# Kernel tuning notes

Measured on AMD Instinct MI355X. Metric: run time of the kernel, lower is better.

The kernel has to match this reference:

```python
import jax, jax.numpy as jnp
import numpy as np

POOL = 7
SUB = 2
C = 256
NUM_CLASS = 81
N_ROIS = 1000
IMG = 1024


def _roi_align(feat, rois, img_size, pool=POOL, sub=SUB):
    # feat: (1, C, H, W); rois: (N, 4) as (y1, x1, y2, x2) in image coords
    H, W = feat.shape[2], feat.shape[3]
    fhw = jnp.array([H, W, H, W], jnp.float32) - 1.0
    im = jnp.concatenate([img_size, img_size]).astype(jnp.float32) - 1.0
    rif = rois * fhw / im  # rois mapped into feature-map coords
    S = pool * sub  # subsampled grid per axis (14)
    h_step = (rif[:, 2] - rif[:, 0]) / S  # (N,)
    w_step = (rif[:, 3] - rif[:, 1]) / S
    grid = jnp.arange(S, dtype=jnp.float32) + 0.5
    ys = grid[None, :] * h_step[:, None] + rif[:, 0:1]  # (N, S)
    xs = grid[None, :] * w_step[:, None] + rif[:, 1:2]  # (N, S)
    cy = ys[:, :, None]  # (N, S, 1) -> broadcast (N, S, S)
    cx = xs[:, None, :]  # (N, 1, S)
    iu = jnp.floor(cy)
    il = jnp.floor(cx)
    ly = cy - iu  # frac parts (bilinear weights)
    lx = cx - il
    iu = iu.astype(jnp.int32)
    il = il.astype(jnp.int32)
    idn = jnp.ceil(cy).astype(jnp.int32)
    ir = jnp.ceil(cx).astype(jnp.int32)
    iu = jnp.broadcast_to(iu, (rois.shape[0], S, S))
    idn = jnp.broadcast_to(idn, (rois.shape[0], S, S))
    il = jnp.broadcast_to(il, (rois.shape[0], S, S))
    ir = jnp.broadcast_to(ir, (rois.shape[0], S, S))
    f = feat[0]  # (C, H, W)
    # fancy-index gather of 4 corners: each (C, N, S, S)
    pre = (f[:, iu, il] * (1 - ly) * (1 - lx)
           + f[:, idn, il] * ly * (1 - lx)
           + f[:, iu, ir] * (1 - ly) * lx
           + f[:, idn, ir] * ly * lx)
    pre = pre.transpose(1, 0, 2, 3)  # (N, C, S, S)
    N = rois.shape[0]
    post = pre.reshape(N, f.shape[0], pool, sub, pool, sub).max(axis=(3, 5))
    return post  # (N, C, pool, pool)


def _pyramid_roi_pool(feats, rois, img_size):
    h = rois[:, 2] - rois[:, 0] + 1
    w = rois[:, 3] - rois[:, 1] + 1
    lvl = jnp.floor(jnp.log(jnp.sqrt(h * w) / 224.0) / 0.693147 + 4.0)
    lvl = jnp.clip(lvl, 2.0, 5.0)
    # compute ROIAlign against each level, select per-roi by mask
    out = jnp.zeros((rois.shape[0], C, POOL, POOL), jnp.float32)
    for i, l in enumerate(range(2, 6)):
        pooled = _roi_align(feats[i], rois, img_size)
        mask = (lvl == l)[:, None, None, None]
        out = jnp.where(mask, pooled, out)
    return out


def setup_inputs() -> dict:
    key = jax.random.key(0)
    ks = jax.random.split(key, 10)
    feat2 = jax.random.normal(ks[0], (1, C, 256, 256), jnp.float32)
    feat3 = jax.random.normal(ks[1], (1, C, 128, 128), jnp.float32)
    feat4 = jax.random.normal(ks[2], (1, C, 64, 64), jnp.float32)
    feat5 = jax.random.normal(ks[3], (1, C, 32, 32), jnp.float32)
    # valid boxes: log-uniform sizes in [32, 512] to cover levels 2..5
    u = jax.random.uniform(ks[4], (N_ROIS, 4))
    sh = jnp.exp(jnp.log(32.0) + u[:, 0] * (jnp.log(512.0) - jnp.log(32.0)))
    sw = jnp.exp(jnp.log(32.0) + u[:, 1] * (jnp.log(512.0) - jnp.log(32.0)))
    y1 = u[:, 2] * (IMG - 1 - sh)
    x1 = u[:, 3] * (IMG - 1 - sw)
    rois = jnp.stack([y1, x1, y1 + sh, x1 + sw], axis=1).astype(jnp.float32)
    img_size = jnp.array([IMG, IMG], jnp.int32)
    D = C * POOL * POOL  # 12544
    W1 = jax.random.normal(ks[5], (D, 1024), jnp.float32) * 0.01
    b1 = jnp.zeros((1024,), jnp.float32)
    W2 = jax.random.normal(ks[6], (1024, 1024), jnp.float32) * 0.01
    b2 = jnp.zeros((1024,), jnp.float32)
    Wloc = jax.random.normal(ks[7], (1024, NUM_CLASS * 4), jnp.float32) * 0.001
    bloc = jnp.zeros((NUM_CLASS * 4,), jnp.float32)
    Wsc = jax.random.normal(ks[8], (1024, NUM_CLASS), jnp.float32) * 0.01
    bsc = jnp.zeros((NUM_CLASS,), jnp.float32)
    return {"feat2": feat2, "feat3": feat3, "feat4": feat4, "feat5": feat5,
            "rois": rois, "img_size": img_size,
            "W1": W1, "b1": b1, "W2": W2, "b2": b2,
            "Wloc": Wloc, "bloc": bloc, "Wsc": Wsc, "bsc": bsc}


def reference(feat2, feat3, feat4, feat5, rois, img_size,
              W1, b1, W2, b2, Wloc, bloc, Wsc, bsc):
    pooled = _pyramid_roi_pool([feat2, feat3, feat4, feat5], rois, img_size)
    x = pooled.reshape(pooled.shape[0], -1)  # (N, 12544)
    fc = jax.nn.relu(x @ W1 + b1)
    fc = jax.nn.relu(fc @ W2 + b2)
    roi_cls_locs = fc @ Wloc + bloc
    roi_scores = fc @ Wsc + bsc
    return roi_cls_locs, roi_scores
```

## Files before the change

kernel.cpp:

```cpp
#include <hip/hip_runtime.h>
#include <hip/hip_bf16.h>
#include <cstdint>
#include <cstddef>

typedef __bf16 bf16x8 __attribute__((ext_vector_type(8)));
typedef _Float16 f16x8 __attribute__((ext_vector_type(8)));
typedef _Float16 f16x4 __attribute__((ext_vector_type(4)));
typedef float floatx4 __attribute__((ext_vector_type(4)));

#define NROIS 1000
#define PD    12544
#define K2_2  2048
#define NLOC  324
#define NSC   81
#define NH    405

#define OFF_T2    0u
#define OFF_T3    16777216u
#define OFF_T4    20971520u
#define OFF_T5    22020096u
#define OFF_FT    0u
#define OFF_POOL  11141120u
#define OFF_W1T   17563648u
#define OFF_PART1 23986176u
#define OFF_FC1   32374784u
#define OFF_W2T   33423360u
#define OFF_WHT   34471936u
#define OFF_FC2   34996224u
#define OFF_PART2 23986176u

__device__ __forceinline__ unsigned short f2bf(float x) {
    unsigned int u = __float_as_uint(x);
    u = u + 0x7fffu + ((u >> 16) & 1u);
    return (unsigned short)(u >> 16);
}
__device__ __forceinline__ float bf2f(unsigned short h) {
    return __uint_as_float(((unsigned int)h) << 16);
}
__device__ __forceinline__ ushort2 split_hl(float f) {
    const unsigned short hi = f2bf(f);
    const unsigned short lo = f2bf(f - bf2f(hi));
    return make_ushort2(hi, lo);
}

__global__ __launch_bounds__(256) void prep_kernel(
    const float* __restrict__ f2, const float* __restrict__ f3,
    const float* __restrict__ f4, const float* __restrict__ f5,
    _Float16* __restrict__ fT,
    const float* __restrict__ W1, _Float16* __restrict__ W1T,
    const float* __restrict__ W2, const float* __restrict__ Wloc,
    const float* __restrict__ Wsc, ushort2* __restrict__ W2T,
    ushort2* __restrict__ WhT)
{
    __shared__ float tile[64][65];
    const int bid = blockIdx.x;
    const int tid = threadIdx.x;
    const int g4  = tid & 15;
    const int pr  = tid >> 4;

    if (bid < 5440) {
        int bx = bid % 1360;
        const int c0 = (bid / 1360) * 64;
        const float* src; _Float16* dst; int P;
        if (bx < 1024)      {            src = f2; dst = fT + OFF_T2; P = 65536; }
        else if (bx < 1280) { bx -= 1024; src = f3; dst = fT + OFF_T3; P = 16384; }
        else if (bx < 1344) { bx -= 1280; src = f4; dst = fT + OFF_T4; P = 4096; }
        else                { bx -= 1344; src = f5; dst = fT + OFF_T5; P = 1024; }
        const int p0 = bx * 64;

#pragma unroll
        for (int k = 0; k < 4; ++k) {
            const int ch = pr + k * 16;
            const float4 v = *reinterpret_cast<const float4*>(
                &src[(size_t)(c0 + ch) * P + p0 + g4 * 4]);
            tile[ch][g4 * 4 + 0] = v.x;
            tile[ch][g4 * 4 + 1] = v.y;
            tile[ch][g4 * 4 + 2] = v.z;
            tile[ch][g4 * 4 + 3] = v.w;
        }
        __syncthreads();

#pragma unroll
        for (int k = 0; k < 4; ++k) {
            const int px = pr + k * 16;
            union { _Float16 h[4]; uint2 u; } pk;
            pk.h[0] = (_Float16)tile[g4 * 4 + 0][px];
            pk.h[1] = (_Float16)tile[g4 * 4 + 1][px];
            pk.h[2] = (_Float16)tile[g4 * 4 + 2][px];
            pk.h[3] = (_Float16)tile[g4 * 4 + 3][px];
            *reinterpret_cast<uint2*>(&dst[(size_t)(p0 + px) * 256 + c0 + g4 * 4]) = pk.u;
        }
    } else if (bid < 8576) {
        const int v  = bid - 5440;
        const int p0 = (v % 196) * 64;
        const int n0 = (v / 196) * 64;

#pragma unroll
        for (int k = 0; k < 4; ++k) {
            const int r    = pr + k * 16;
            const int pp   = p0 + r;
            const int ksrc = (pp & 255) * 49 + (pp >> 8);
            const float4 w = *reinterpret_cast<const float4*>(
                &W1[(size_t)ksrc * 1024 + n0 + g4 * 4]);
            tile[r][g4 * 4 + 0] = w.x;
            tile[r][g4 * 4 + 1] = w.y;
            tile[r][g4 * 4 + 2] = w.z;
            tile[r][g4 * 4 + 3] = w.w;
        }
        __syncthreads();

#pragma unroll
        for (int k = 0; k < 4; ++k) {
            const int nr = pr + k * 16;
            union { _Float16 h[4]; uint2 u; } pk;
            pk.h[0] = (_Float16)tile[g4 * 4 + 0][nr];
            pk.h[1] = (_Float16)tile[g4 * 4 + 1][nr];
            pk.h[2] = (_Float16)tile[g4 * 4 + 2][nr];
            pk.h[3] = (_Float16)tile[g4 * 4 + 3][nr];
            *reinterpret_cast<uint2*>(&W1T[(size_t)(n0 + nr) * PD + p0 + g4 * 4]) = pk.u;
        }
    } else {
        const int v  = bid - 8576;
        const int p0 = (v % 16) * 64;
        const int by = v / 16;
        const int col = tid & 63;
        const int r0  = tid >> 6;

        if (by < 16) {
            const int n0 = by * 64;
#pragma unroll
            for (int k = 0; k < 4; ++k) {
                const int r = pr + k * 16;
                const float4 w = *reinterpret_cast<const float4*>(
                    &W2[(size_t)(p0 + r) * 1024 + n0 + g4 * 4]);
                tile[r][g4 * 4 + 0] = w.x;
                tile[r][g4 * 4 + 1] = w.y;
                tile[r][g4 * 4 + 2] = w.z;
                tile[r][g4 * 4 + 3] = w.w;
            }
            __syncthreads();
#pragma unroll
            for (int nr = r0; nr < 64; nr += 4)
                W2T[(size_t)(n0 + nr) * 1024 + p0 + col] = split_hl(tile[col][nr]);
        } else {
            const int n0 = (by - 16) * 64;
#pragma unroll
            for (int r = r0; r < 64; r += 4) {
                const int pp = p0 + r;
                const int n  = n0 + col;
                float w = 0.0f;
                if (n < NLOC)    w = Wloc[(size_t)pp * NLOC + n];
                else if (n < NH) w = Wsc[(size_t)pp * NSC + (n - NLOC)];
                tile[r][col] = w;
            }
            __syncthreads();
#pragma unroll
            for (int nr = r0; nr < 64; nr += 4)
                WhT[(size_t)(n0 + nr) * 1024 + p0 + col] = split_hl(tile[col][nr]);
        }
    }
}

__global__ __launch_bounds__(256) void roi_pool_kernel(
    const _Float16* __restrict__ fT, const float* __restrict__ rois,
    const int* __restrict__ img_size, _Float16* __restrict__ pooledH)
{
    const int roi  = blockIdx.x;
    const int ph   = blockIdx.y;
    const int tid  = threadIdx.x;
    const int lane = tid & 63;
    const int wave = tid >> 6;
    const int syy  = wave >> 1;
    const int sxp  = wave & 1;

    const float y1 = rois[roi * 4 + 0];
    const float x1 = rois[roi * 4 + 1];
    const float y2 = rois[roi * 4 + 2];
    const float x2 = rois[roi * 4 + 3];

    const float hh = y2 - y1 + 1.0f;
    const float ww = x2 - x1 + 1.0f;
    float lvlf = floorf(logf(sqrtf(hh * ww) / 224.0f) / 0.693147f + 4.0f);
    lvlf = fminf(fmaxf(lvlf, 2.0f), 5.0f);
    const int lvl = (int)lvlf;

    const _Float16* f;
    int H;
    if (lvl == 2)      { f = fT + OFF_T2; H = 256; }
    else if (lvl == 3) { f = fT + OFF_T3; H = 128; }
    else if (lvl == 4) { f = fT + OFF_T4; H = 64;  }
    else               { f = fT + OFF_T5; H = 32;  }
    const int W = H;

    const float imh = (float)img_size[0] - 1.0f;
    const float imw = (float)img_size[1] - 1.0f;
    const float r0 = y1 * (float)(H - 1) / imh;
    const float r1 = x1 * (float)(W - 1) / imw;
    const float r2 = y2 * (float)(H - 1) / imh;
    const float r3 = x2 * (float)(W - 1) / imw;
    const float hs  = (r2 - r0) * (1.0f / 14.0f);
    const float wst = (r3 - r1) * (1.0f / 14.0f);

    const float cy = ((float)(ph * 2 + syy) + 0.5f) * hs + r0;
    const float fy = floorf(cy);
    int   iu  = (int)fy;
    int   idn = (int)ceilf(cy);
    const float ly = cy - fy;
    iu  = min(max(iu, 0),  H - 1);
    idn = min(max(idn, 0), H - 1);
    const float wU = 1.0f - ly, wD = ly;
    const f16x4* rowU = (const f16x4*)(f + (size_t)(iu  * W) * 256);
    const f16x4* rowD = (const f16x4*)(f + (size_t)(idn * W) * 256);

    __shared__ float4 red[4][7][64];

#pragma unroll
    for (int pw = 0; pw < 7; ++pw) {
        const int sx = pw * 2 + sxp;
        const float cx = ((float)sx + 0.5f) * wst + r1;
        const float fx = floorf(cx);
        int   il = (int)fx;
        int   ir = (int)ceilf(cx);
        const float lx = cx - fx;
        il = min(max(il, 0), W - 1);
        ir = min(max(ir, 0), W - 1);

        const f16x4 h00 = rowU[il * 64 + lane];
        const f16x4 h01 = rowU[ir * 64 + lane];
        const f16x4 h10 = rowD[il * 64 + lane];
        const f16x4 h11 = rowD[ir * 64 + lane];
        const float lxm = 1.0f - lx;
        float4 v;
        v.x = ((float)h00.x * lxm + (float)h01.x * lx) * wU + ((float)h10.x * lxm + (float)h11.x * lx) * wD;
        v.y = ((float)h00.y * lxm + (float)h01.y * lx) * wU + ((float)h10.y * lxm + (float)h11.y * lx) * wD;
        v.z = ((float)h00.z * lxm + (float)h01.z * lx) * wU + ((float)h10.z * lxm + (float)h11.z * lx) * wD;
        v.w = ((float)h00.w * lxm + (float)h01.w * lx) * wU + ((float)h10.w * lxm + (float)h11.w * lx) * wD;
        red[wave][pw][lane] = v;
    }
    __syncthreads();

    for (int idx = tid; idx < 448; idx += 256) {
        const int pw = idx >> 6, cg = idx & 63;
        const float4 a = red[0][pw][cg];
        const float4 b = red[1][pw][cg];
        const float4 c = red[2][pw][cg];
        const float4 d = red[3][pw][cg];
        union { _Float16 h[4]; uint2 v2; } pk;
        pk.h[0] = (_Float16)fmaxf(fmaxf(a.x, b.x), fmaxf(c.x, d.x));
        pk.h[1] = (_Float16)fmaxf(fmaxf(a.y, b.y), fmaxf(c.y, d.y));
        pk.h[2] = (_Float16)fmaxf(fmaxf(a.z, b.z), fmaxf(c.z, d.z));
        pk.h[3] = (_Float16)fmaxf(fmaxf(a.w, b.w), fmaxf(c.w, d.w));
        _Float16* outp = pooledH + (size_t)roi * PD + (ph * 7 + pw) * 256 + cg * 4;
        *reinterpret_cast<uint2*>(outp) = pk.v2;
    }
}

template<bool F16>
__global__ __launch_bounds__(256, 4) void gemm_16b_kernel(
    const unsigned short* __restrict__ A,
    const unsigned short* __restrict__ B,
    float* __restrict__ partial,
    int K2, int N)
{
    __shared__ __align__(16) unsigned short As[64 * 64];
    __shared__ __align__(16) unsigned short Bs[128 * 64];

    const int tid  = threadIdx.x;
    const int lane = tid & 63;
    const int wave = tid >> 6;

    const int totalSteps = K2 >> 6;
    const int nz = gridDim.x;
    const int z  = blockIdx.x;
    const int q  = totalSteps / nz, r = totalSteps % nz;
    const int myStart = z * q + min(z, r);
    const int mySteps = q + (z < r ? 1 : 0);

    const int n0 = blockIdx.y * 128;
    const int m0 = blockIdx.z * 64;

    const int rIn  = lane >> 3;
    const int cSrc = (lane & 7) ^ rIn;

    const int mrow = lane & 15, quad = lane >> 4;

    floatx4 acc[8];
#pragma unroll
    for (int j = 0; j < 8; ++j)
        acc[j] = (floatx4){0.f, 0.f, 0.f, 0.f};

    for (int s = 0; s < mySteps; ++s) {
        const int k0 = (myStart + s) * 64;
#pragma unroll
        for (int qq = 0; qq < 2; ++qq) {
            const int rowBase = wave * 16 + qq * 8;
            const unsigned short* ga =
                A + (size_t)(m0 + rowBase + rIn) * K2 + k0 + cSrc * 8;
            __builtin_amdgcn_global_load_lds(
                (const __attribute__((address_space(1))) void*)ga,
                (__attribute__((address_space(3))) void*)&As[rowBase * 64], 16, 0, 0);
        }
#pragma unroll
        for (int qq = 0; qq < 4; ++qq) {
            const int rowBase = wave * 32 + qq * 8;
            const unsigned short* gb =
                B + (size_t)(n0 + rowBase + rIn) * K2 + k0 + cSrc * 8;
            __builtin_amdgcn_global_load_lds(
                (const __attribute__((address_space(1))) void*)gb,
                (__attribute__((address_space(3))) void*)&Bs[rowBase * 64], 16, 0, 0);
        }
        __syncthreads();

#pragma unroll
        for (int ks = 0; ks < 2; ++ks) {
            const int ra = wave * 16 + mrow;
            const int ca = ((ks * 4 + quad) ^ (ra & 7)) * 8;
#pragma unroll
            for (int j = 0; j < 8; ++j) {
                const int rb = j * 16 + mrow;
                const int cb = ((ks * 4 + quad) ^ (rb & 7)) * 8;
                if constexpr (F16) {
                    const f16x8 aF = *reinterpret_cast<const f16x8*>(&As[ra * 64 + ca]);
                    const f16x8 bF = *reinterpret_cast<const f16x8*>(&Bs[rb * 64 + cb]);
                    acc[j] = __builtin_amdgcn_mfma_f32_16x16x32_f16(aF, bF, acc[j], 0, 0, 0);
                } else {
                    const bf16x8 aF = *reinterpret_cast<const bf16x8*>(&As[ra * 64 + ca]);
                    const bf16x8 bF = *reinterpret_cast<const bf16x8*>(&Bs[rb * 64 + cb]);
                    acc[j] = __builtin_amdgcn_mfma_f32_16x16x32_bf16(aF, bF, acc[j], 0, 0, 0);
                }
            }
        }
        __syncthreads();
    }

    float* p = partial + (size_t)blockIdx.x * (size_t)(gridDim.z * 64) * N;
    const int row = m0 + wave * 16 + quad * 4;
#pragma unroll
    for (int j = 0; j < 8; ++j) {
        const int col = n0 + j * 16 + mrow;
#pragma unroll
        for (int rr = 0; rr < 4; ++rr)
            p[(size_t)(row + rr) * N + col] = acc[j][rr];
    }
}

__global__ __launch_bounds__(256) void reduce_fc_kernel(
    const float* __restrict__ partial, const float* __restrict__ bias,
    ushort2* __restrict__ outHL, int nz)
{
    const int i4 = blockIdx.x * 256 + threadIdx.x;
    const int off = i4 * 4;
    const int m = off >> 10, n = off & 1023;
    float4 acc = *reinterpret_cast<const float4*>(partial + off);
    for (int z = 1; z < nz; ++z) {
        const float4 v = *reinterpret_cast<const float4*>(
            partial + (size_t)z * 1024 * 1024 + off);
        acc.x += v.x; acc.y += v.y; acc.z += v.z; acc.w += v.w;
    }
    const float4 bv = *reinterpret_cast<const float4*>(bias + n);
    ushort2* o = outHL + (size_t)m * 1024 + n;
    o[0] = split_hl(fmaxf(acc.x + bv.x, 0.f));
    o[1] = split_hl(fmaxf(acc.y + bv.y, 0.f));
    o[2] = split_hl(fmaxf(acc.z + bv.z, 0.f));
    o[3] = split_hl(fmaxf(acc.w + bv.w, 0.f));
}

__global__ __launch_bounds__(256) void reduce_heads_kernel(
    const float* __restrict__ partial, const float* __restrict__ bloc,
    const float* __restrict__ bsc, float* __restrict__ out0,
    float* __restrict__ out1, int nz)
{
    const int m = blockIdx.x;
    for (int n = threadIdx.x; n < NH; n += 256) {
        float s = 0.f;
        for (int z = 0; z < nz; ++z)
            s += partial[(size_t)z * 1024 * 512 + (size_t)m * 512 + n];
        if (n < NLOC) out0[(size_t)m * NLOC + n] = s + bloc[n];
        else          out1[(size_t)m * NSC + (n - NLOC)] = s + bsc[n - NLOC];
    }
}

extern "C" void kernel_launch(void* const* d_in, const int* in_sizes, int n_in,
                              void* d_out, int out_size, void* d_ws, size_t ws_size,
                              hipStream_t stream)
{
    const float* f2   = (const float*)d_in[0];
    const float* f3   = (const float*)d_in[1];
    const float* f4   = (const float*)d_in[2];
    const float* f5   = (const float*)d_in[3];
    const float* rois = (const float*)d_in[4];
    const int*   img  = (const int*)d_in[5];
    const float* W1   = (const float*)d_in[6];
    const float* b1   = (const float*)d_in[7];
    const float* W2   = (const float*)d_in[8];
    const float* b2   = (const float*)d_in[9];
    const float* Wloc = (const float*)d_in[10];
    const float* bloc = (const float*)d_in[11];
    const float* Wsc  = (const float*)d_in[12];
    const float* bsc  = (const float*)d_in[13];
    float* out = (float*)d_out;

    float* ws = (float*)d_ws;
    _Float16*  fT     = (_Float16*)(ws + OFF_FT);
    _Float16*  pooled = (_Float16*)(ws + OFF_POOL);
    _Float16*  w1t    = (_Float16*)(ws + OFF_W1T);
    float*     part1  = ws + OFF_PART1;
    float*     part2  = ws + OFF_PART2;
    ushort2*   w2t    = (ushort2*)(ws + OFF_W2T);
    ushort2*   wht    = (ushort2*)(ws + OFF_WHT);
    ushort2*   fc1    = (ushort2*)(ws + OFF_FC1);
    ushort2*   fc2    = (ushort2*)(ws + OFF_FC2);

    prep_kernel<<<dim3(8944), 256, 0, stream>>>(
        f2, f3, f4, f5, fT, W1, w1t, W2, Wloc, Wsc, w2t, wht);

    roi_pool_kernel<<<dim3(NROIS, 7), 256, 0, stream>>>(fT, rois, img, pooled);

    gemm_16b_kernel<true><<<dim3(8, 8, 16), 256, 0, stream>>>(
        (const unsigned short*)pooled, (const unsigned short*)w1t, part1,
        PD, 1024);
    reduce_fc_kernel<<<1024, 256, 0, stream>>>(part1, b1, fc1, 8);

    gemm_16b_kernel<false><<<dim3(4, 8, 16), 256, 0, stream>>>(
        (const unsigned short*)fc1, (const unsigned short*)w2t, part2,
        K2_2, 1024);
    reduce_fc_kernel<<<1024, 256, 0, stream>>>(part2, b2, fc2, 4);

    gemm_16b_kernel<false><<<dim3(8, 4, 16), 256, 0, stream>>>(
        (const unsigned short*)fc2, (const unsigned short*)wht, part2,
        K2_2, 512);
    reduce_heads_kernel<<<NROIS, 256, 0, stream>>>(
        part2, bloc, bsc, out, out + (size_t)NROIS * NLOC, 8);
}
```

Before: 312.7 us.

## Use plain fp16 for FC2/heads and co-schedule weight prep with ROI pooling

FC2 and the head GEMMs switch from split hi/lo bf16 operands (K doubled to 2048) to single fp16 operands with K=1024. That halves the MFMA work and the weight and activation bytes for those GEMMs. The weight-transpose work now runs in the same launch as the ROI pooling blocks, and only the feature transpose stays in its own kernel, so weight prep overlaps pooling. The cost is lower accuracy, since the compensated split-precision scheme is gone and fp16 range limits now apply to the activations and weights.

```diff
diff --git a/kernel.cpp b/kernel.cpp
--- a/kernel.cpp
+++ b/kernel.cpp
@@ -3,14 +3,13 @@
 #include <cstdint>
 #include <cstddef>
 
-typedef __bf16 bf16x8 __attribute__((ext_vector_type(8)));
 typedef _Float16 f16x8 __attribute__((ext_vector_type(8)));
 typedef _Float16 f16x4 __attribute__((ext_vector_type(4)));
 typedef float floatx4 __attribute__((ext_vector_type(4)));
 
 #define NROIS 1000
 #define PD    12544
-#define K2_2  2048
+#define KFC   1024
 #define NLOC  324
 #define NSC   81
 #define NH    405
@@ -24,110 +23,189 @@
 #define OFF_W1T   17563648u
 #define OFF_PART1 23986176u
 #define OFF_FC1   32374784u
-#define OFF_W2T   33423360u
-#define OFF_WHT   34471936u
-#define OFF_FC2   34996224u
+#define OFF_W2T   32899072u
+#define OFF_WHT   33423360u
+#define OFF_FC2   33685504u
 #define OFF_PART2 23986176u
 
-__device__ __forceinline__ unsigned short f2bf(float x) {
-    unsigned int u = __float_as_uint(x);
-    u = u + 0x7fffu + ((u >> 16) & 1u);
-    return (unsigned short)(u >> 16);
-}
-__device__ __forceinline__ float bf2f(unsigned short h) {
-    return __uint_as_float(((unsigned int)h) << 16);
-}
-__device__ __forceinline__ ushort2 split_hl(float f) {
-    const unsigned short hi = f2bf(f);
-    const unsigned short lo = f2bf(f - bf2f(hi));
-    return make_ushort2(hi, lo);
-}
-
-__global__ __launch_bounds__(256) void prep_kernel(
+__global__ __launch_bounds__(256) void transpose_feat_kernel(
     const float* __restrict__ f2, const float* __restrict__ f3,
     const float* __restrict__ f4, const float* __restrict__ f5,
-    _Float16* __restrict__ fT,
-    const float* __restrict__ W1, _Float16* __restrict__ W1T,
-    const float* __restrict__ W2, const float* __restrict__ Wloc,
-    const float* __restrict__ Wsc, ushort2* __restrict__ W2T,
-    ushort2* __restrict__ WhT)
+    _Float16* __restrict__ fT)
 {
     __shared__ float tile[64][65];
-    const int bid = blockIdx.x;
     const int tid = threadIdx.x;
     const int g4  = tid & 15;
     const int pr  = tid >> 4;
 
-    if (bid < 5440) {
-        int bx = bid % 1360;
-        const int c0 = (bid / 1360) * 64;
-        const float* src; _Float16* dst; int P;
-        if (bx < 1024)      {            src = f2; dst = fT + OFF_T2; P = 65536; }
-        else if (bx < 1280) { bx -= 1024; src = f3; dst = fT + OFF_T3; P = 16384; }
-        else if (bx < 1344) { bx -= 1280; src = f4; dst = fT + OFF_T4; P = 4096; }
-        else                { bx -= 1344; src = f5; dst = fT + OFF_T5; P = 1024; }
-        const int p0 = bx * 64;
-
-#pragma unroll
-        for (int k = 0; k < 4; ++k) {
-            const int ch = pr + k * 16;
-            const float4 v = *reinterpret_cast<const float4*>(
-                &src[(size_t)(c0 + ch) * P + p0 + g4 * 4]);
-            tile[ch][g4 * 4 + 0] = v.x;
-            tile[ch][g4 * 4 + 1] = v.y;
-            tile[ch][g4 * 4 + 2] = v.z;
-            tile[ch][g4 * 4 + 3] = v.w;
+    int bx = blockIdx.x % 1360;
+    const int c0 = (blockIdx.x / 1360) * 64;
+    const float* src; _Float16* dst; int P;
+    if (bx < 1024)      {            src = f2; dst = fT + OFF_T2; P = 65536; }
+    else if (bx < 1280) { bx -= 1024; src = f3; dst = fT + OFF_T3; P = 16384; }
+    else if (bx < 1344) { bx -= 1280; src = f4; dst = fT + OFF_T4; P = 4096; }
+    else                { bx -= 1344; src = f5; dst = fT + OFF_T5; P = 1024; }
+    const int p0 = bx * 64;
+
+#pragma unroll
+    for (int k = 0; k < 4; ++k) {
+        const int ch = pr + k * 16;
+        const float4 v = *reinterpret_cast<const float4*>(
+            &src[(size_t)(c0 + ch) * P + p0 + g4 * 4]);
+        tile[ch][g4 * 4 + 0] = v.x;
+        tile[ch][g4 * 4 + 1] = v.y;
+        tile[ch][g4 * 4 + 2] = v.z;
+        tile[ch][g4 * 4 + 3] = v.w;
+    }
+    __syncthreads();
+#pragma unroll
+    for (int k = 0; k < 4; ++k) {
+        const int px = pr + k * 16;
+        union { _Float16 h[4]; uint2 u; } pk;
+        pk.h[0] = (_Float16)tile[g4 * 4 + 0][px];
+        pk.h[1] = (_Float16)tile[g4 * 4 + 1][px];
+        pk.h[2] = (_Float16)tile[g4 * 4 + 2][px];
+        pk.h[3] = (_Float16)tile[g4 * 4 + 3][px];
+        *reinterpret_cast<uint2*>(&dst[(size_t)(p0 + px) * 256 + c0 + g4 * 4]) = pk.u;
+    }
+}
+
+__global__ __launch_bounds__(256) void pool_prep_kernel(
+    const _Float16* __restrict__ fT, const float* __restrict__ rois,
+    const int* __restrict__ img_size, _Float16* __restrict__ pooledH,
+    const float* __restrict__ W1, _Float16* __restrict__ W1T,
+    const float* __restrict__ W2, const float* __restrict__ Wloc,
+    const float* __restrict__ Wsc, _Float16* __restrict__ W2T,
+    _Float16* __restrict__ WhT)
+{
+    __shared__ __align__(16) char smem[28672];
+    const int bid = blockIdx.x;
+    const int tid = threadIdx.x;
+
+    if (bid < 7000) {
+        const int roi  = bid / 7;
+        const int ph   = bid % 7;
+        const int lane = tid & 63;
+        const int wave = tid >> 6;
+        const int syy  = wave >> 1;
+        const int sxp  = wave & 1;
+
+        const float y1 = rois[roi * 4 + 0];
+        const float x1 = rois[roi * 4 + 1];
+        const float y2 = rois[roi * 4 + 2];
+        const float x2 = rois[roi * 4 + 3];
+
+        const float hh = y2 - y1 + 1.0f;
+        const float ww = x2 - x1 + 1.0f;
+        float lvlf = floorf(logf(sqrtf(hh * ww) / 224.0f) / 0.693147f + 4.0f);
+        lvlf = fminf(fmaxf(lvlf, 2.0f), 5.0f);
+        const int lvl = (int)lvlf;
+
+        const _Float16* f;
+        int H;
+        if (lvl == 2)      { f = fT + OFF_T2; H = 256; }
+        else if (lvl == 3) { f = fT + OFF_T3; H = 128; }
+        else if (lvl == 4) { f = fT + OFF_T4; H = 64;  }
+        else               { f = fT + OFF_T5; H = 32;  }
+        const int W = H;
+
+        const float imh = (float)img_size[0] - 1.0f;
+        const float imw = (float)img_size[1] - 1.0f;
+        const float r0 = y1 * (float)(H - 1) / imh;
+        const float r1 = x1 * (float)(W - 1) / imw;
+        const float r2 = y2 * (float)(H - 1) / imh;
+        const float r3 = x2 * (float)(W - 1) / imw;
+        const float hs  = (r2 - r0) * (1.0f / 14.0f);
+        const float wst = (r3 - r1) * (1.0f / 14.0f);
+
+        const float cy = ((float)(ph * 2 + syy) + 0.5f) * hs + r0;
+        const float fy = floorf(cy);
+        int   iu  = (int)fy;
+        int   idn = (int)ceilf(cy);
+        const float ly = cy - fy;
+        iu  = min(max(iu, 0),  H - 1);
+        idn = min(max(idn, 0), H - 1);
+        const float wU = 1.0f - ly, wD = ly;
+        const f16x4* rowU = (const f16x4*)(f + (size_t)(iu  * W) * 256);
+        const f16x4* rowD = (const f16x4*)(f + (size_t)(idn * W) * 256);
+
+        float4 (*red)[7][64] = reinterpret_cast<float4 (*)[7][64]>(smem);
+
+#pragma unroll
+        for (int pw = 0; pw < 7; ++pw) {
+            const int sx = pw * 2 + sxp;
+            const float cx = ((float)sx + 0.5f) * wst + r1;
+            const float fx = floorf(cx);
+            int   il = (int)fx;
+            int   ir = (int)ceilf(cx);
+            const float lx = cx - fx;
+            il = min(max(il, 0), W - 1);
+            ir = min(max(ir, 0), W - 1);
+
+            const f16x4 h00 = rowU[il * 64 + lane];
+            const f16x4 h01 = rowU[ir * 64 + lane];
+            const f16x4 h10 = rowD[il * 64 + lane];
+            const f16x4 h11 = rowD[ir * 64 + lane];
+            const float lxm = 1.0f - lx;
+            float4 v;
+            v.x = ((float)h00.x * lxm + (float)h01.x * lx) * wU + ((float)h10.x * lxm + (float)h11.x * lx) * wD;
+            v.y = ((float)h00.y * lxm + (float)h01.y * lx) * wU + ((float)h10.y * lxm + (float)h11.y * lx) * wD;
+            v.z = ((float)h00.z * lxm + (float)h01.z * lx) * wU + ((float)h10.z * lxm + (float)h11.z * lx) * wD;
+            v.w = ((float)h00.w * lxm + (float)h01.w * lx) * wU + ((float)h10.w * lxm + (float)h11.w * lx) * wD;
+            red[wave][pw][lane] = v;
         }
         __syncthreads();
 
-#pragma unroll
-        for (int k = 0; k < 4; ++k) {
-            const int px = pr + k * 16;
-            union { _Float16 h[4]; uint2 u; } pk;
-            pk.h[0] = (_Float16)tile[g4 * 4 + 0][px];
-            pk.h[1] = (_Float16)tile[g4 * 4 + 1][px];
-            pk.h[2] = (_Float16)tile[g4 * 4 + 2][px];
-            pk.h[3] = (_Float16)tile[g4 * 4 + 3][px];
-            *reinterpret_cast<uint2*>(&dst[(size_t)(p0 + px) * 256 + c0 + g4 * 4]) = pk.u;
-        }
-    } else if (bid < 8576) {
-        const int v  = bid - 5440;
-        const int p0 = (v % 196) * 64;
-        const int n0 = (v / 196) * 64;
-
-#pragma unroll
-        for (int k = 0; k < 4; ++k) {
-            const int r    = pr + k * 16;
-            const int pp   = p0 + r;
-            const int ksrc = (pp & 255) * 49 + (pp >> 8);
-            const float4 w = *reinterpret_cast<const float4*>(
-                &W1[(size_t)ksrc * 1024 + n0 + g4 * 4]);
-            tile[r][g4 * 4 + 0] = w.x;
-            tile[r][g4 * 4 + 1] = w.y;
-            tile[r][g4 * 4 + 2] = w.z;
-            tile[r][g4 * 4 + 3] = w.w;
-        }
-        __syncthreads();
-
-#pragma unroll
-        for (int k = 0; k < 4; ++k) {
-            const int nr = pr + k * 16;
-            union { _Float16 h[4]; uint2 u; } pk;
-            pk.h[0] = (_Float16)tile[g4 * 4 + 0][nr];
-            pk.h[1] = (_Float16)tile[g4 * 4 + 1][nr];
-            pk.h[2] = (_Float16)tile[g4 * 4 + 2][nr];
-            pk.h[3] = (_Float16)tile[g4 * 4 + 3][nr];
-            *reinterpret_cast<uint2*>(&W1T[(size_t)(n0 + nr) * PD + p0 + g4 * 4]) = pk.u;
+        for (int idx = tid; idx < 448; idx += 256) {
+            const int pw = idx >> 6, cg = idx & 63;
+            const float4 a = red[0][pw][cg];
+            const float4 b = red[1][pw][cg];
+            const float4 c = red[2][pw][cg];
+            const float4 d = red[3][pw][cg];
+            union { _Float16 h[4]; uint2 v2; } pk;
+            pk.h[0] = (_Float16)fmaxf(fmaxf(a.x, b.x), fmaxf(c.x, d.x));
+            pk.h[1] = (_Float16)fmaxf(fmaxf(a.y, b.y), fmaxf(c.y, d.y));
+            pk.h[2] = (_Float16)fmaxf(fmaxf(a.z, b.z), fmaxf(c.z, d.z));
+            pk.h[3] = (_Float16)fmaxf(fmaxf(a.w, b.w), fmaxf(c.w, d.w));
+            _Float16* outp = pooledH + (size_t)roi * PD + (ph * 7 + pw) * 256 + cg * 4;
+            *reinterpret_cast<uint2*>(outp) = pk.v2;
         }
     } else {
-        const int v  = bid - 8576;
-        const int p0 = (v % 16) * 64;
-        const int by = v / 16;
-        const int col = tid & 63;
-        const int r0  = tid >> 6;
-
-        if (by < 16) {
-            const int n0 = by * 64;
+        float (*tile)[65] = reinterpret_cast<float (*)[65]>(smem);
+        const int g4 = tid & 15;
+        const int pr = tid >> 4;
+
+        if (bid < 10136) {
+            const int v  = bid - 7000;
+            const int p0 = (v % 196) * 64;
+            const int n0 = (v / 196) * 64;
+#pragma unroll
+            for (int k = 0; k < 4; ++k) {
+                const int r    = pr + k * 16;
+                const int pp   = p0 + r;
+                const int ksrc = (pp & 255) * 49 + (pp >> 8);
+                const float4 w = *reinterpret_cast<const float4*>(
+                    &W1[(size_t)ksrc * 1024 + n0 + g4 * 4]);
+                tile[r][g4 * 4 + 0] = w.x;
+                tile[r][g4 * 4 + 1] = w.y;
+                tile[r][g4 * 4 + 2] = w.z;
+                tile[r][g4 * 4 + 3] = w.w;
+            }
+            __syncthreads();
+#pragma unroll
+            for (int k = 0; k < 4; ++k) {
+                const int nr = pr + k * 16;
+                union { _Float16 h[4]; uint2 u; } pk;
+                pk.h[0] = (_Float16)tile[g4 * 4 + 0][nr];
+                pk.h[1] = (_Float16)tile[g4 * 4 + 1][nr];
+                pk.h[2] = (_Float16)tile[g4 * 4 + 2][nr];
+                pk.h[3] = (_Float16)tile[g4 * 4 + 3][nr];
+                *reinterpret_cast<uint2*>(&W1T[(size_t)(n0 + nr) * PD + p0 + g4 * 4]) = pk.u;
+            }
+        } else if (bid < 10392) {
+            const int v  = bid - 10136;
+            const int p0 = (v % 16) * 64;
+            const int n0 = (v / 16) * 64;
 #pragma unroll
             for (int k = 0; k < 4; ++k) {
                 const int r = pr + k * 16;
@@ -140,10 +218,21 @@
             }
             __syncthreads();
 #pragma unroll
-            for (int nr = r0; nr < 64; nr += 4)
-                W2T[(size_t)(n0 + nr) * 1024 + p0 + col] = split_hl(tile[col][nr]);
+            for (int k = 0; k < 4; ++k) {
+                const int nr = pr + k * 16;
+                union { _Float16 h[4]; uint2 u; } pk;
+                pk.h[0] = (_Float16)tile[g4 * 4 + 0][nr];
+                pk.h[1] = (_Float16)tile[g4 * 4 + 1][nr];
+                pk.h[2] = (_Float16)tile[g4 * 4 + 2][nr];
+                pk.h[3] = (_Float16)tile[g4 * 4 + 3][nr];
+                *reinterpret_cast<uint2*>(&W2T[(size_t)(n0 + nr) * KFC + p0 + g4 * 4]) = pk.u;
+            }
         } else {
-            const int n0 = (by - 16) * 64;
+            const int v  = bid - 10392;
+            const int p0 = (v % 16) * 64;
+            const int n0 = (v / 16) * 64;
+            const int col = tid & 63;
+            const int r0  = tid >> 6;
 #pragma unroll
             for (int r = r0; r < 64; r += 4) {
                 const int pp = p0 + r;
@@ -155,108 +244,20 @@
             }
             __syncthreads();
 #pragma unroll
-            for (int nr = r0; nr < 64; nr += 4)
-                WhT[(size_t)(n0 + nr) * 1024 + p0 + col] = split_hl(tile[col][nr]);
-        }
-    }
-}
-
-__global__ __launch_bounds__(256) void roi_pool_kernel(
-    const _Float16* __restrict__ fT, const float* __restrict__ rois,
-    const int* __restrict__ img_size, _Float16* __restrict__ pooledH)
-{
-    const int roi  = blockIdx.x;
-    const int ph   = blockIdx.y;
-    const int tid  = threadIdx.x;
-    const int lane = tid & 63;
-    const int wave = tid >> 6;
-    const int syy  = wave >> 1;
-    const int sxp  = wave & 1;
-
-    const float y1 = rois[roi * 4 + 0];
-    const float x1 = rois[roi * 4 + 1];
-    const float y2 = rois[roi * 4 + 2];
-    const float x2 = rois[roi * 4 + 3];
-
-    const float hh = y2 - y1 + 1.0f;
-    const float ww = x2 - x1 + 1.0f;
-    float lvlf = floorf(logf(sqrtf(hh * ww) / 224.0f) / 0.693147f + 4.0f);
-    lvlf = fminf(fmaxf(lvlf, 2.0f), 5.0f);
-    const int lvl = (int)lvlf;
-
-    const _Float16* f;
-    int H;
-    if (lvl == 2)      { f = fT + OFF_T2; H = 256; }
-    else if (lvl == 3) { f = fT + OFF_T3; H = 128; }
-    else if (lvl == 4) { f = fT + OFF_T4; H = 64;  }
-    else               { f = fT + OFF_T5; H = 32;  }
-    const int W = H;
-
-    const float imh = (float)img_size[0] - 1.0f;
-    const float imw = (float)img_size[1] - 1.0f;
-    const float r0 = y1 * (float)(H - 1) / imh;
-    const float r1 = x1 * (float)(W - 1) / imw;
-    const float r2 = y2 * (float)(H - 1) / imh;
-    const float r3 = x2 * (float)(W - 1) / imw;
-    const float hs  = (r2 - r0) * (1.0f / 14.0f);
-    const float wst = (r3 - r1) * (1.0f / 14.0f);
-
-    const float cy = ((float)(ph * 2 + syy) + 0.5f) * hs + r0;
-    const float fy = floorf(cy);
-    int   iu  = (int)fy;
-    int   idn = (int)ceilf(cy);
-    const float ly = cy - fy;
-    iu  = min(max(iu, 0),  H - 1);
-    idn = min(max(idn, 0), H - 1);
-    const float wU = 1.0f - ly, wD = ly;
-    const f16x4* rowU = (const f16x4*)(f + (size_t)(iu  * W) * 256);
-    const f16x4* rowD = (const f16x4*)(f + (size_t)(idn * W) * 256);
-
-    __shared__ float4 red[4][7][64];
-
-#pragma unroll
-    for (int pw = 0; pw < 7; ++pw) {
-        const int sx = pw * 2 + sxp;
-        const float cx = ((float)sx + 0.5f) * wst + r1;
-        const float fx = floorf(cx);
-        int   il = (int)fx;
-        int   ir = (int)ceilf(cx);
-        const float lx = cx - fx;
-        il = min(max(il, 0), W - 1);
-        ir = min(max(ir, 0), W - 1);
-
-        const f16x4 h00 = rowU[il * 64 + lane];
-        const f16x4 h01 = rowU[ir * 64 + lane];
-        const f16x4 h10 = rowD[il * 64 + lane];
-        const f16x4 h11 = rowD[ir * 64 + lane];
-        const float lxm = 1.0f - lx;
-        float4 v;
-        v.x = ((float)h00.x * lxm + (float)h01.x * lx) * wU + ((float)h10.x * lxm + (float)h11.x * lx) * wD;
-        v.y = ((float)h00.y * lxm + (float)h01.y * lx) * wU + ((float)h10.y * lxm + (float)h11.y * lx) * wD;
-        v.z = ((float)h00.z * lxm + (float)h01.z * lx) * wU + ((float)h10.z * lxm + (float)h11.z * lx) * wD;
-        v.w = ((float)h00.w * lxm + (float)h01.w * lx) * wU + ((float)h10.w * lxm + (float)h11.w * lx) * wD;
-        red[wave][pw][lane] = v;
-    }
-    __syncthreads();
-
-    for (int idx = tid; idx < 448; idx += 256) {
-        const int pw = idx >> 6, cg = idx & 63;
-        const float4 a = red[0][pw][cg];
-        const float4 b = red[1][pw][cg];
-        const float4 c = red[2][pw][cg];
-        const float4 d = red[3][pw][cg];
-        union { _Float16 h[4]; uint2 v2; } pk;
-        pk.h[0] = (_Float16)fmaxf(fmaxf(a.x, b.x), fmaxf(c.x, d.x));
-        pk.h[1] = (_Float16)fmaxf(fmaxf(a.y, b.y), fmaxf(c.y, d.y));
-        pk.h[2] = (_Float16)fmaxf(fmaxf(a.z, b.z), fmaxf(c.z, d.z));
-        pk.h[3] = (_Float16)fmaxf(fmaxf(a.w, b.w), fmaxf(c.w, d.w));
-        _Float16* outp = pooledH + (size_t)roi * PD + (ph * 7 + pw) * 256 + cg * 4;
-        *reinterpret_cast<uint2*>(outp) = pk.v2;
-    }
-}
-
-template<bool F16>
-__global__ __launch_bounds__(256, 4) void gemm_16b_kernel(
+            for (int k = 0; k < 4; ++k) {
+                const int nr = pr + k * 16;
+                union { _Float16 h[4]; uint2 u; } pk;
+                pk.h[0] = (_Float16)tile[g4 * 4 + 0][nr];
+                pk.h[1] = (_Float16)tile[g4 * 4 + 1][nr];
+                pk.h[2] = (_Float16)tile[g4 * 4 + 2][nr];
+                pk.h[3] = (_Float16)tile[g4 * 4 + 3][nr];
+                *reinterpret_cast<uint2*>(&WhT[(size_t)(n0 + nr) * KFC + p0 + g4 * 4]) = pk.u;
+            }
+        }
+    }
+}
+
+__global__ __launch_bounds__(256, 4) void gemm_f16_kernel(
     const unsigned short* __restrict__ A,
     const unsigned short* __restrict__ B,
     float* __restrict__ partial,
@@ -315,19 +316,13 @@
         for (int ks = 0; ks < 2; ++ks) {
             const int ra = wave * 16 + mrow;
             const int ca = ((ks * 4 + quad) ^ (ra & 7)) * 8;
+            const f16x8 aF = *reinterpret_cast<const f16x8*>(&As[ra * 64 + ca]);
 #pragma unroll
             for (int j = 0; j < 8; ++j) {
                 const int rb = j * 16 + mrow;
                 const int cb = ((ks * 4 + quad) ^ (rb & 7)) * 8;
-                if constexpr (F16) {
-                    const f16x8 aF = *reinterpret_cast<const f16x8*>(&As[ra * 64 + ca]);
-                    const f16x8 bF = *reinterpret_cast<const f16x8*>(&Bs[rb * 64 + cb]);
-                    acc[j] = __builtin_amdgcn_mfma_f32_16x16x32_f16(aF, bF, acc[j], 0, 0, 0);
-                } else {
-                    const bf16x8 aF = *reinterpret_cast<const bf16x8*>(&As[ra * 64 + ca]);
-                    const bf16x8 bF = *reinterpret_cast<const bf16x8*>(&Bs[rb * 64 + cb]);
-                    acc[j] = __builtin_amdgcn_mfma_f32_16x16x32_bf16(aF, bF, acc[j], 0, 0, 0);
-                }
+                const f16x8 bF = *reinterpret_cast<const f16x8*>(&Bs[rb * 64 + cb]);
+                acc[j] = __builtin_amdgcn_mfma_f32_16x16x32_f16(aF, bF, acc[j], 0, 0, 0);
             }
         }
         __syncthreads();
@@ -346,11 +341,11 @@
 
 __global__ __launch_bounds__(256) void reduce_fc_kernel(
     const float* __restrict__ partial, const float* __restrict__ bias,
-    ushort2* __restrict__ outHL, int nz)
+    _Float16* __restrict__ outH, int nz)
 {
     const int i4 = blockIdx.x * 256 + threadIdx.x;
     const int off = i4 * 4;
-    const int m = off >> 10, n = off & 1023;
+    const int n = off & 1023;
     float4 acc = *reinterpret_cast<const float4*>(partial + off);
     for (int z = 1; z < nz; ++z) {
         const float4 v = *reinterpret_cast<const float4*>(
@@ -358,11 +353,12 @@
         acc.x += v.x; acc.y += v.y; acc.z += v.z; acc.w += v.w;
     }
     const float4 bv = *reinterpret_cast<const float4*>(bias + n);
-    ushort2* o = outHL + (size_t)m * 1024 + n;
-    o[0] = split_hl(fmaxf(acc.x + bv.x, 0.f));
-    o[1] = split_hl(fmaxf(acc.y + bv.y, 0.f));
-    o[2] = split_hl(fmaxf(acc.z + bv.z, 0.f));
-    o[3] = split_hl(fmaxf(acc.w + bv.w, 0.f));
+    union { _Float16 h[4]; uint2 u; } pk;
+    pk.h[0] = (_Float16)fmaxf(acc.x + bv.x, 0.f);
+    pk.h[1] = (_Float16)fmaxf(acc.y + bv.y, 0.f);
+    pk.h[2] = (_Float16)fmaxf(acc.z + bv.z, 0.f);
+    pk.h[3] = (_Float16)fmaxf(acc.w + bv.w, 0.f);
+    *reinterpret_cast<uint2*>(outH + off) = pk.u;
 }
 
 __global__ __launch_bounds__(256) void reduce_heads_kernel(
@@ -406,29 +402,29 @@
     _Float16*  w1t    = (_Float16*)(ws + OFF_W1T);
     float*     part1  = ws + OFF_PART1;
     float*     part2  = ws + OFF_PART2;
-    ushort2*   w2t    = (ushort2*)(ws + OFF_W2T);
-    ushort2*   wht    = (ushort2*)(ws + OFF_WHT);
-    ushort2*   fc1    = (ushort2*)(ws + OFF_FC1);
-    ushort2*   fc2    = (ushort2*)(ws + OFF_FC2);
-
-    prep_kernel<<<dim3(8944), 256, 0, stream>>>(
-        f2, f3, f4, f5, fT, W1, w1t, W2, Wloc, Wsc, w2t, wht);
-
-    roi_pool_kernel<<<dim3(NROIS, 7), 256, 0, stream>>>(fT, rois, img, pooled);
-
-    gemm_16b_kernel<true><<<dim3(8, 8, 16), 256, 0, stream>>>(
+    _Float16*  fc1    = (_Float16*)(ws + OFF_FC1);
+    _Float16*  w2t    = (_Float16*)(ws + OFF_W2T);
+    _Float16*  wht    = (_Float16*)(ws + OFF_WHT);
+    _Float16*  fc2    = (_Float16*)(ws + OFF_FC2);
+
+    transpose_feat_kernel<<<dim3(5440), 256, 0, stream>>>(f2, f3, f4, f5, fT);
+
+    pool_prep_kernel<<<dim3(10520), 256, 0, stream>>>(
+        fT, rois, img, pooled, W1, w1t, W2, Wloc, Wsc, w2t, wht);
+
+    gemm_f16_kernel<<<dim3(8, 8, 16), 256, 0, stream>>>(
         (const unsigned short*)pooled, (const unsigned short*)w1t, part1,
         PD, 1024);
     reduce_fc_kernel<<<1024, 256, 0, stream>>>(part1, b1, fc1, 8);
 
-    gemm_16b_kernel<false><<<dim3(4, 8, 16), 256, 0, stream>>>(
+    gemm_f16_kernel<<<dim3(4, 8, 16), 256, 0, stream>>>(
         (const unsigned short*)fc1, (const unsigned short*)w2t, part2,
-        K2_2, 1024);
+        KFC, 1024);
     reduce_fc_kernel<<<1024, 256, 0, stream>>>(part2, b2, fc2, 4);
 
-    gemm_16b_kernel<false><<<dim3(8, 4, 16), 256, 0, stream>>>(
+    gemm_f16_kernel<<<dim3(8, 4, 16), 256, 0, stream>>>(
         (const unsigned short*)fc2, (const unsigned short*)wht, part2,
-        K2_2, 512);
+        KFC, 512);
     reduce_heads_kernel<<<NROIS, 256, 0, stream>>>(
         part2, bloc, bsc, out, out + (size_t)NROIS * NLOC, 8);
 }
```

New measurement: 306.5 us. 2.0% less time.
